# Kernel optimization log

Hardware: AMD Instinct MI355X
Metric: run time of the kernel (lower is better)

The kernel has to match this reference:

```python
import jax, jax.numpy as jnp
import numpy as np

# static config (matches init_kwargs)
H = 64; W = 64; WS = 8; SHIFT = 4; HEADS = 16; DIM = 512; TED = 512; B = 16
NW = (H // WS) * (W // WS)          # 64 windows
WS2 = WS * WS                        # 64 tokens per window
N = WS2 + 1                          # +1 time-embedding token appended per window
HIDDEN = int(DIM * 4.0)


def _rel_pos_index():
    # standard Swin relative-position index over the WS*WS window tokens
    coords = np.stack(np.meshgrid(np.arange(WS), np.arange(WS), indexing='ij'))  # (2, WS, WS)
    cf = coords.reshape(2, -1)
    rel = (cf[:, :, None] - cf[:, None, :]).transpose(1, 2, 0)  # (WS2, WS2, 2)
    rel[..., 0] += WS - 1
    rel[..., 1] += WS - 1
    rel[..., 0] *= 2 * WS - 1
    return rel.sum(-1)  # (WS2, WS2) int


def _attn_mask():
    # shifted-window attention mask, exactly as built in __init__
    img_mask = np.zeros((H, W), dtype=np.float32)
    slices = (slice(0, -WS), slice(-WS, -SHIFT), slice(-SHIFT, None))
    cnt = 0
    for hs in slices:
        for ws_ in slices:
            img_mask[hs, ws_] = cnt
            cnt += 1
    mw = img_mask.reshape(H // WS, WS, W // WS, WS).transpose(0, 2, 1, 3).reshape(-1, WS2)  # (NW, WS2)
    diff = mw[:, None, :] - mw[:, :, None]
    return np.where(diff != 0, -100.0, 0.0).astype(np.float32)  # (NW, WS2, WS2)


def _ln(x, g, b):
    m = x.mean(-1, keepdims=True)
    v = ((x - m) ** 2).mean(-1, keepdims=True)
    return (x - m) / jnp.sqrt(v + 1e-5) * g + b


def setup_inputs() -> dict:
    key = jax.random.key(0)
    ks = jax.random.split(key, 10)
    s = 0.02
    return {
        'x': jax.random.normal(ks[0], (B, H * W, DIM), dtype=jnp.float32),
        'emb': jax.random.normal(ks[1], (B, TED), dtype=jnp.float32),
        'gamma1': jnp.ones((DIM,), jnp.float32),
        'beta1': jnp.zeros((DIM,), jnp.float32),
        'W_emb': jax.random.normal(ks[2], (TED, DIM), jnp.float32) * s,
        'b_emb': jnp.zeros((DIM,), jnp.float32),
        'W_qkv': jax.random.normal(ks[3], (DIM, 3 * DIM), jnp.float32) * s,
        'b_qkv': jnp.zeros((3 * DIM,), jnp.float32),
        'rel_bias_table': jax.random.normal(ks[4], ((2 * WS - 1) ** 2, HEADS), jnp.float32) * s,
        'W_proj': jax.random.normal(ks[5], (DIM, DIM), jnp.float32) * s,
        'b_proj': jnp.zeros((DIM,), jnp.float32),
        'gamma2': jnp.ones((DIM,), jnp.float32),
        'beta2': jnp.zeros((DIM,), jnp.float32),
        'W1': jax.random.normal(ks[6], (DIM, HIDDEN), jnp.float32) * s,
        'b1': jnp.zeros((HIDDEN,), jnp.float32),
        'W2': jax.random.normal(ks[7], (HIDDEN, DIM), jnp.float32) * s,
        'b2': jnp.zeros((DIM,), jnp.float32),
    }


def reference(x, emb, gamma1, beta1, W_emb, b_emb, W_qkv, b_qkv, rel_bias_table,
              W_proj, b_proj, gamma2, beta2, W1, b1, W2, b2):
    Bb, L, C = x.shape
    hd = C // HEADS
    shortcut = x
    # norm1 -> spatial -> cyclic shift
    xn = _ln(x, gamma1, beta1).reshape(Bb, H, W, C)
    xs = jnp.roll(xn, (-SHIFT, -SHIFT), axis=(1, 2))
    # window partition: (B, NW, WS2, C)
    xw = xs.reshape(Bb, H // WS, WS, W // WS, WS, C).transpose(0, 1, 3, 2, 4, 5)
    xw = xw.reshape(Bb, NW, WS2, C)
    # append time-embedding token to each window
    t = jax.nn.silu(emb) @ W_emb + b_emb                       # (B, C)
    t = jnp.broadcast_to(t[:, None, None, :], (Bb, NW, 1, C))
    xw = jnp.concatenate([xw, t], axis=2).reshape(Bb * NW, N, C)
    # windowed multi-head attention
    qkv = (xw @ W_qkv + b_qkv).reshape(Bb * NW, N, 3, HEADS, hd).transpose(2, 0, 3, 1, 4)
    q, k, v = qkv[0] * (hd ** -0.5), qkv[1], qkv[2]            # (B*NW, HEADS, N, hd)
    attn = jnp.einsum('bhnd,bhmd->bhnm', q, k)
    bias = rel_bias_table[_rel_pos_index().reshape(-1)].reshape(WS2, WS2, HEADS).transpose(2, 0, 1)
    bias = jnp.pad(bias, ((0, 0), (0, 1), (0, 1)))             # zero bias for time token
    attn = attn + bias[None]
    mask = jnp.pad(jnp.asarray(_attn_mask()), ((0, 0), (0, 1), (0, 1)))  # (NW, N, N)
    attn = attn.reshape(Bb, NW, HEADS, N, N) + mask[None, :, None]
    attn = jax.nn.softmax(attn.reshape(Bb * NW, HEADS, N, N), axis=-1)
    out = jnp.einsum('bhnm,bhmd->bnhd', attn, v).reshape(Bb * NW, N, C)
    out = (out @ W_proj + b_proj)[:, :WS2]                     # drop time token
    # window reverse + reverse shift
    out = out.reshape(Bb, H // WS, W // WS, WS, WS, C).transpose(0, 1, 3, 2, 4, 5).reshape(Bb, H, W, C)
    out = jnp.roll(out, (SHIFT, SHIFT), axis=(1, 2)).reshape(Bb, L, C)
    x1 = shortcut + out
    # norm2 + MLP (exact GELU, as torch nn.GELU default)
    hmid = jax.nn.gelu(_ln(x1, gamma2, beta2) @ W1 + b1, approximate=False)
    return x1 + hmid @ W2 + b2
```

## Files before the change

### kernel.cpp

```cpp
#include <hip/hip_runtime.h>
#include <hip/hip_bf16.h>

typedef __hip_bfloat16 bf16;
typedef short short4_t __attribute__((ext_vector_type(4)));
typedef short short8 __attribute__((ext_vector_type(8)));
typedef float f32x4 __attribute__((ext_vector_type(4)));

#define DIMC 512
#define HEADS_ 16
#define NTOK 65
#define NWIN 64
#define NB 16
#define HID 2048
#define TOTROWS 66560
#define ATT_CHUNK_WB 128
#define ATT_CHUNK_ROWS (ATT_CHUNK_WB * NTOK)


__device__ __forceinline__ float b2f(short s) {
  unsigned int u = ((unsigned int)(unsigned short)s) << 16;
  float f; __builtin_memcpy(&f, &u, 4); return f;
}
__device__ __forceinline__ short f2s(float f) {
  bf16 b = __float2bfloat16(f);
  short s; __builtin_memcpy(&s, &b, 2); return s;
}

__device__ __forceinline__ void async_lds16(const bf16* g, bf16* l) {
  __builtin_amdgcn_global_load_lds(
      (const __attribute__((address_space(1))) unsigned int*)g,
      (__attribute__((address_space(3))) unsigned int*)l,
      16, 0, 0);
}

__device__ __forceinline__ void wave_stats512(const float* v, float& m, float& rstd)
{
  float s = 0.0f, ss = 0.0f;
  #pragma unroll
  for (int e = 0; e < 8; ++e) { s += v[e]; ss += v[e] * v[e]; }
  #pragma unroll
  for (int o = 1; o < 64; o <<= 1) { s += __shfl_xor(s, o); ss += __shfl_xor(ss, o); }
  m = s * (1.0f / 512.0f);
  rstd = rsqrtf(ss * (1.0f / 512.0f) - m * m + 1e-5f);
}

__device__ __forceinline__ float gelu_t(float v) {
  float u = v + 0.044715f * v * v * v;
  float z2 = 1.5957691216f * fabsf(u);
  float t = __expf(-z2);
  float th = 1.0f - 2.0f * t / (1.0f + t);
  th = (u < 0.0f) ? -th : th;
  return 0.5f * v * (1.0f + th);
}


__global__ __launch_bounds__(256) void time_emb_kernel(
    const float* __restrict__ emb, const float* __restrict__ W_emb,
    const float* __restrict__ b_emb, float* __restrict__ t)
{
  int b = blockIdx.x;
  int c = blockIdx.y * 256 + threadIdx.x;
  __shared__ float se[512];
  for (int k = threadIdx.x; k < 512; k += 256) {
    float e = emb[b * 512 + k];
    se[k] = e / (1.0f + expf(-e));
  }
  __syncthreads();
  float acc = b_emb[c];
  for (int k = 0; k < 512; ++k) acc += se[k] * W_emb[k * 512 + c];
  t[b * 512 + c] = acc;
}

__global__ void transpose_cast_kernel(const float* __restrict__ W, bf16* __restrict__ Wt,
                                      int Kd, int Nd)
{
  __shared__ float tile[32][33];
  int n0 = blockIdx.x * 32, k0 = blockIdx.y * 32;
  for (int r = threadIdx.y; r < 32; r += 8)
    tile[r][threadIdx.x] = W[(long)(k0 + r) * Nd + n0 + threadIdx.x];
  __syncthreads();
  for (int r = threadIdx.y; r < 32; r += 8)
    Wt[(long)(n0 + r) * Kd + k0 + threadIdx.x] = __float2bfloat16(tile[threadIdx.x][r]);
}

__global__ __launch_bounds__(256) void bias_mask_kernel(
    const float* __restrict__ btab, float* __restrict__ tbl)
{
  int h = blockIdx.x, wt = blockIdx.y;
  for (int idx = threadIdx.x; idx < 6400; idx += 256) {
    int i = idx / 80, t = idx % 80;
    float v;
    if (t >= 65) v = -1e30f;
    else if (i >= 64 || t == 64) v = 0.0f;
    else {
      int rel = (((i >> 3) - (t >> 3) + 7) * 15) + ((i & 7) - (t & 7) + 7);
      v = btab[rel * HEADS_ + h];
      int rci = (wt & 2) ? (((i >> 3) < 4) ? 1 : 2) : 0;
      int cci = (wt & 1) ? (((i & 7) < 4) ? 1 : 2) : 0;
      int rct = (wt & 2) ? (((t >> 3) < 4) ? 1 : 2) : 0;
      int cct = (wt & 1) ? (((t & 7) < 4) ? 1 : 2) : 0;
      if (rci * 3 + cci != rct * 3 + cct) v -= 100.0f;
    }
    tbl[(h * 4 + wt) * 6400 + idx] = v;
  }
}

__global__ __launch_bounds__(256) void ln1_window_kernel(
    const float* __restrict__ x, const float* __restrict__ gamma,
    const float* __restrict__ beta, const float* __restrict__ t,
    bf16* __restrict__ xw)
{
  long r = (long)blockIdx.x * 4 + (threadIdx.x >> 6);
  int lane = threadIdx.x & 63;
  int wb = (int)(r / NTOK), i = (int)(r % NTOK);
  int b = wb >> 6, w = wb & 63;
  bf16* out = xw + r * 512 + lane * 8;
  if (i == 64) {
    const float* tr = t + b * 512 + lane * 8;
    short8 o;
    #pragma unroll
    for (int e = 0; e < 8; ++e) o[e] = f2s(tr[e]);
    *(short8*)out = o;
    return;
  }
  int wh = w >> 3, ww = w & 7, ih = i >> 3, iw = i & 7;
  int hsrc = ((wh * 8 + ih) + 4) & 63;
  int wsrc = ((ww * 8 + iw) + 4) & 63;
  const float* xr = x + ((long)b * 4096 + hsrc * 64 + wsrc) * 512 + lane * 8;
  float v[8];
  *(f32x4*)&v[0] = *(const f32x4*)xr;
  *(f32x4*)&v[4] = *(const f32x4*)(xr + 4);
  float m, rstd;
  wave_stats512(v, m, rstd);
  const float* g = gamma + lane * 8;
  const float* bt = beta + lane * 8;
  short8 o;
  #pragma unroll
  for (int e = 0; e < 8; ++e) o[e] = f2s((v[e] - m) * rstd * g[e] + bt[e]);
  *(short8*)out = o;
}

__global__ __launch_bounds__(256) void ln2_kernel(
    const float* __restrict__ x1, const float* __restrict__ gamma,
    const float* __restrict__ beta, bf16* __restrict__ out)
{
  long r = (long)blockIdx.x * 4 + (threadIdx.x >> 6);
  int lane = threadIdx.x & 63;
  const float* xr = x1 + r * 512 + lane * 8;
  float v[8];
  *(f32x4*)&v[0] = *(const f32x4*)xr;
  *(f32x4*)&v[4] = *(const f32x4*)(xr + 4);
  float m, rstd;
  wave_stats512(v, m, rstd);
  const float* g = gamma + lane * 8;
  const float* bt = beta + lane * 8;
  short8 o;
  #pragma unroll
  for (int e = 0; e < 8; ++e) o[e] = f2s((v[e] - m) * rstd * g[e] + bt[e]);
  *(short8*)(out + r * 512 + lane * 8) = o;
}

template<int EPI>
__global__ __launch_bounds__(512, 4) void gemmk_kernel(
    const bf16* __restrict__ A, const bf16* __restrict__ Bt,
    const float* __restrict__ bias, int N, int K, int nx,
    bf16* __restrict__ outB, float* __restrict__ outF,
    const float* __restrict__ xin, int rowOffset)
{
  __shared__ bf16 lA[3][128 * 32];
  __shared__ bf16 lB[3][256 * 32];
  const int tid = threadIdx.x;
  const int lane = tid & 63, wv = tid >> 6;
  const int wm = wv >> 2, wn = wv & 3;
  const int fr = lane & 15, fg = lane >> 4;

  const int nwg = gridDim.x, bid = blockIdx.x;
  const int q = nwg >> 3, rr8 = nwg & 7;
  const int xcd = bid & 7, idx = bid >> 3;
  const int sid = (xcd < rr8 ? xcd * (q + 1) : rr8 * (q + 1) + (xcd - rr8) * q) + idx;
  const long row0 = (long)(sid / nx) * 128;
  const long col0 = (long)(sid % nx) * 256;

  const int rl = lane >> 2, sp = lane & 3;
  const int s = sp ^ ((rl >> 1) & 3);
  const bf16* gA  = A  + (row0 + wv * 16 + rl) * (long)K + s * 8;
  const bf16* gB0 = Bt + (col0 + wv * 16 + rl) * (long)K + s * 8;
  const bf16* gB1 = Bt + (col0 + 128 + wv * 16 + rl) * (long)K + s * 8;

  f32x4 acc[4][4] = {};
  const int nkt = K >> 5;
  const int swr = (fg ^ ((fr >> 1) & 3)) << 4;

  auto stage = [&](int buf, int kt) {
    async_lds16(gA + kt, &lA[buf][wv * 512]);
    async_lds16(gB0 + kt, &lB[buf][wv * 512]);
    async_lds16(gB1 + kt, &lB[buf][4096 + wv * 512]);
  };

  stage(0, 0);
  stage(1, 32);

  for (int t = 0; t < nkt; ++t) {
    if (t + 1 < nkt)
      asm volatile("s_waitcnt vmcnt(3)" ::: "memory");
    else
      asm volatile("s_waitcnt vmcnt(0)" ::: "memory");
    __builtin_amdgcn_s_barrier();
    const int buf = t % 3;
    short8 af[4], bfv[4];
    #pragma unroll
    for (int mi = 0; mi < 4; ++mi)
      af[mi] = *(const short8*)((const char*)&lA[buf][0] + (wm * 64 + mi * 16 + fr) * 64 + swr);
    #pragma unroll
    for (int ni = 0; ni < 4; ++ni)
      bfv[ni] = *(const short8*)((const char*)&lB[buf][0] + (wn * 64 + ni * 16 + fr) * 64 + swr);
    if (t + 2 < nkt) stage((t + 2) % 3, (t + 2) << 5);
    __builtin_amdgcn_s_setprio(1);
    #pragma unroll
    for (int mi = 0; mi < 4; ++mi)
      #pragma unroll
      for (int ni = 0; ni < 4; ++ni)
        acc[mi][ni] = __builtin_amdgcn_mfma_f32_16x16x32_bf16(af[mi], bfv[ni], acc[mi][ni], 0, 0, 0);
    __builtin_amdgcn_s_setprio(0);
  }

  float bs[4];
  #pragma unroll
  for (int ni = 0; ni < 4; ++ni) bs[ni] = bias[col0 + wn * 64 + ni * 16 + fr];
  #pragma unroll
  for (int mi = 0; mi < 4; ++mi) {
    #pragma unroll
    for (int j = 0; j < 4; ++j) {
      long rr = row0 + wm * 64 + mi * 16 + fg * 4 + j;
      if (EPI == 2) {
        int grow = rowOffset + (int)rr;
        int ii = grow % NTOK;
        if (ii == 64) continue;
        int wb = grow / NTOK;
        int b = wb >> 6, w = wb & 63;
        int wh = w >> 3, ww = w & 7, ih = ii >> 3, iw = ii & 7;
        int hh   = ((wh * 8 + ih) + 4) & 63;
        int wcol = ((ww * 8 + iw) + 4) & 63;
        long orow = ((long)b * 4096 + hh * 64 + wcol) * 512;
        #pragma unroll
        for (int ni = 0; ni < 4; ++ni) {
          long o = orow + col0 + wn * 64 + ni * 16 + fr;
          outF[o] = xin[o] + acc[mi][ni][j] + bs[ni];
        }
      } else {
        #pragma unroll
        for (int ni = 0; ni < 4; ++ni) {
          long cc = col0 + wn * 64 + ni * 16 + fr;
          float v = acc[mi][ni][j] + bs[ni];
          if (EPI == 0) {
            outB[rr * N + cc] = __float2bfloat16(v);
          } else if (EPI == 1) {
            outB[rr * N + cc] = __float2bfloat16(gelu_t(v));
          } else {
            long o = rr * N + cc;
            outF[o] = outF[o] + v;
          }
        }
      }
    }
  }
}

__global__ __launch_bounds__(64, 2) void attn_mfma_kernel(
    const bf16* __restrict__ qkv, bf16* __restrict__ attnO,
    const float* __restrict__ tbl, int wb0)
{
  __shared__ bf16 P[80 * 104];
  const int lwb = blockIdx.x, h = blockIdx.y;
  const int lane = threadIdx.x;
  const int fr = lane & 15, g = lane >> 4;
  const float scale = 0.17677669529663687f;
  const bf16* base = qkv + (long)lwb * 65 * 1536 + h * 32 + g * 8;

  for (int idx = lane; idx < 240; idx += 64) {
    int i = idx / 3, sl = idx % 3;
    *(short8*)&P[i * 104 + 80 + sl * 8] = (short8){0, 0, 0, 0, 0, 0, 0, 0};
  }

  short8 bq[5];
  #pragma unroll
  for (int tn = 0; tn < 5; ++tn) {
    int qr = tn * 16 + fr; qr = qr > 64 ? 64 : qr;
    bq[tn] = *(const short8*)(base + (long)qr * 1536);
  }

  f32x4 acc[5][5];
  #pragma unroll
  for (int tm = 0; tm < 5; ++tm) {
    int kr = tm * 16 + fr; kr = kr > 64 ? 64 : kr;
    short8 ak = *(const short8*)(base + 512 + (long)kr * 1536);
    #pragma unroll
    for (int tn = 0; tn < 5; ++tn)
      acc[tm][tn] = __builtin_amdgcn_mfma_f32_16x16x32_bf16(
          ak, bq[tn], (f32x4){0.0f, 0.0f, 0.0f, 0.0f}, 0, 0, 0);
  }

  const int w = (wb0 + lwb) & 63;
  const int wt = (((w >> 3) == 7) ? 2 : 0) + (((w & 7) == 7) ? 1 : 0);
  const float* tp = tbl + (h * 4 + wt) * 6400;
  #pragma unroll
  for (int tn = 0; tn < 5; ++tn) {
    const int i = tn * 16 + fr;
    const float* ti = tp + i * 80 + g * 4;
    float m = -3.0e38f;
    #pragma unroll
    for (int tm = 0; tm < 5; ++tm) {
      f32x4 bv = *(const f32x4*)(ti + tm * 16);
      #pragma unroll
      for (int r = 0; r < 4; ++r) {
        float sv = fmaf(acc[tm][tn][r], scale, bv[r]);
        acc[tm][tn][r] = sv;
        m = fmaxf(m, sv);
      }
    }
    m = fmaxf(m, __shfl_xor(m, 16));
    m = fmaxf(m, __shfl_xor(m, 32));
    float l = 0.0f;
    #pragma unroll
    for (int tm = 0; tm < 5; ++tm)
      #pragma unroll
      for (int r = 0; r < 4; ++r) {
        float e = __expf(acc[tm][tn][r] - m);
        acc[tm][tn][r] = e;
        l += e;
      }
    l += __shfl_xor(l, 16);
    l += __shfl_xor(l, 32);
    float inv = 1.0f / l;
    #pragma unroll
    for (int tm = 0; tm < 5; ++tm) {
      short4_t pk;
      #pragma unroll
      for (int r = 0; r < 4; ++r) pk[r] = f2s(acc[tm][tn][r] * inv);
      *(short4_t*)&P[i * 104 + tm * 16 + g * 4] = pk;
    }
  }

  const bf16* vbase = qkv + (long)lwb * 65 * 1536 + 1024 + h * 32;
  f32x4 oacc[2][5] = {};
  #pragma unroll
  for (int kt = 0; kt < 3; ++kt) {
    short8 bp[5];
    #pragma unroll
    for (int tn = 0; tn < 5; ++tn)
      bp[tn] = *(const short8*)&P[(tn * 16 + fr) * 104 + kt * 32 + g * 8];
    #pragma unroll
    for (int ma = 0; ma < 2; ++ma) {
      short8 av;
      #pragma unroll
      for (int e = 0; e < 8; ++e) {
        int vr = kt * 32 + g * 8 + e; vr = vr > 64 ? 64 : vr;
        av[e] = *(const short*)(vbase + (long)vr * 1536 + ma * 16 + fr);
      }
      #pragma unroll
      for (int tn = 0; tn < 5; ++tn)
        oacc[ma][tn] = __builtin_amdgcn_mfma_f32_16x16x32_bf16(
            av, bp[tn], oacc[ma][tn], 0, 0, 0);
    }
  }

  #pragma unroll
  for (int tn = 0; tn < 5; ++tn) {
    int i = tn * 16 + fr;
    if (i < 65) {
      bf16* op = attnO + (long)(lwb * 65 + i) * 512 + h * 32 + g * 4;
      #pragma unroll
      for (int ma = 0; ma < 2; ++ma) {
        short4_t o4;
        #pragma unroll
        for (int r = 0; r < 4; ++r) o4[r] = f2s(oacc[ma][tn][r]);
        *(short4_t*)(op + ma * 16) = o4;
      }
    }
  }
}


extern "C" void kernel_launch(void* const* d_in, const int* in_sizes, int n_in,
                              void* d_out, int out_size, void* d_ws, size_t ws_size,
                              hipStream_t stream)
{
  const float* x      = (const float*)d_in[0];
  const float* emb    = (const float*)d_in[1];
  const float* gamma1 = (const float*)d_in[2];
  const float* beta1  = (const float*)d_in[3];
  const float* W_emb  = (const float*)d_in[4];
  const float* b_emb  = (const float*)d_in[5];
  const float* W_qkv  = (const float*)d_in[6];
  const float* b_qkv  = (const float*)d_in[7];
  const float* btab   = (const float*)d_in[8];
  const float* W_proj = (const float*)d_in[9];
  const float* b_proj = (const float*)d_in[10];
  const float* gamma2 = (const float*)d_in[11];
  const float* beta2  = (const float*)d_in[12];
  const float* W1     = (const float*)d_in[13];
  const float* b1     = (const float*)d_in[14];
  const float* W2     = (const float*)d_in[15];
  const float* b2     = (const float*)d_in[16];
  float* out = (float*)d_out;
  (void)n_in; (void)in_sizes; (void)out_size;

  char* ws = (char*)d_ws;
  size_t off = 0;
  auto alloc = [&](size_t bytes) -> char* {
    char* p = ws + off;
    off += (bytes + 255) & ~(size_t)255;
    return p;
  };
  bf16* wt_qkv  = (bf16*)alloc((size_t)1536 * 512 * 2);
  bf16* wt_proj = (bf16*)alloc((size_t)512 * 512 * 2);
  bf16* wt1     = (bf16*)alloc((size_t)2048 * 512 * 2);
  bf16* wt2     = (bf16*)alloc((size_t)512 * 2048 * 2);
  float* tvec   = (float*)alloc((size_t)16 * 512 * 4);
  float* tbl    = (float*)alloc((size_t)16 * 4 * 6400 * 4);

  const size_t sz_xw    = (size_t)TOTROWS * 512 * 2;
  const size_t sz_qkv   = (size_t)TOTROWS * 1536 * 2;
  const size_t sz_attnO = (size_t)TOTROWS * 512 * 2;
  const bool big = ws_size >= off + sz_xw + sz_qkv + sz_attnO + (4u << 20);

  transpose_cast_kernel<<<dim3(1536 / 32, 512 / 32), dim3(32, 8), 0, stream>>>(W_qkv, wt_qkv, 512, 1536);
  transpose_cast_kernel<<<dim3(512 / 32, 512 / 32),  dim3(32, 8), 0, stream>>>(W_proj, wt_proj, 512, 512);
  transpose_cast_kernel<<<dim3(2048 / 32, 512 / 32), dim3(32, 8), 0, stream>>>(W1, wt1, 512, 2048);
  transpose_cast_kernel<<<dim3(512 / 32, 2048 / 32), dim3(32, 8), 0, stream>>>(W2, wt2, 2048, 512);
  time_emb_kernel<<<dim3(16, 2), 256, 0, stream>>>(emb, W_emb, b_emb, tvec);
  bias_mask_kernel<<<dim3(16, 4), 256, 0, stream>>>(btab, tbl);

  if (big) {
    bf16* xw    = (bf16*)alloc(sz_xw);
    bf16* qkv   = (bf16*)alloc(sz_qkv);
    bf16* attnO = (bf16*)alloc(sz_attnO);
    bf16* ln2b  = xw;
    bf16* h     = qkv;

    ln1_window_kernel<<<TOTROWS / 4, 256, 0, stream>>>(x, gamma1, beta1, tvec, xw);
    gemmk_kernel<0><<<6 * 520, 512, 0, stream>>>(
        xw, wt_qkv, b_qkv, 1536, 512, 6, qkv, nullptr, nullptr, 0);
    attn_mfma_kernel<<<dim3(NB * NWIN, HEADS_), 64, 0, stream>>>(qkv, attnO, tbl, 0);
    gemmk_kernel<2><<<2 * 520, 512, 0, stream>>>(
        attnO, wt_proj, b_proj, 512, 512, 2, nullptr, out, x, 0);
    ln2_kernel<<<65536 / 4, 256, 0, stream>>>(out, gamma2, beta2, ln2b);
    gemmk_kernel<1><<<8 * 512, 512, 0, stream>>>(
        ln2b, wt1, b1, 2048, 512, 8, h, nullptr, nullptr, 0);
    gemmk_kernel<3><<<2 * 512, 512, 0, stream>>>(
        h, wt2, b2, 512, 2048, 2, nullptr, out, nullptr, 0);
  } else {
    char* regionA = alloc(sz_xw);
    bf16* xw   = (bf16*)regionA;
    bf16* ln2b = (bf16*)regionA;
    bf16* qkv_c = (bf16*)alloc((size_t)ATT_CHUNK_ROWS * 1536 * 2);
    char* regionB = alloc(sz_attnO);
    bf16* attnO = (bf16*)regionB;
    bf16* h_c   = (bf16*)regionB;

    ln1_window_kernel<<<TOTROWS / 4, 256, 0, stream>>>(x, gamma1, beta1, tvec, xw);
    for (int ac = 0; ac < 8; ++ac) {
      long r0 = (long)ac * ATT_CHUNK_ROWS;
      gemmk_kernel<0><<<6 * 65, 512, 0, stream>>>(
          xw + r0 * 512, wt_qkv, b_qkv, 1536, 512, 6, qkv_c, nullptr, nullptr, 0);
      attn_mfma_kernel<<<dim3(ATT_CHUNK_WB, HEADS_), 64, 0, stream>>>(
          qkv_c, attnO + r0 * 512, tbl, ac * ATT_CHUNK_WB);
    }
    gemmk_kernel<2><<<2 * 520, 512, 0, stream>>>(
        attnO, wt_proj, b_proj, 512, 512, 2, nullptr, out, x, 0);
    ln2_kernel<<<65536 / 4, 256, 0, stream>>>(out, gamma2, beta2, ln2b);
    for (int mc = 0; mc < 4; ++mc) {
      long r0 = (long)mc * 16384;
      gemmk_kernel<1><<<8 * 128, 512, 0, stream>>>(
          ln2b + r0 * 512, wt1, b1, 2048, 512, 8, h_c, nullptr, nullptr, 0);
      gemmk_kernel<3><<<2 * 128, 512, 0, stream>>>(
          h_c, wt2, b2, 512, 2048, 2, nullptr, out + r0 * 512, nullptr, 0);
    }
  }
}
```

Measured before the change: 879.2 us.

## Use 4 waves per GEMM block with 128x64 per-wave tiles

Reworks the GEMM from 8 waves in a 2x4 layout to 4 waves, each computing a 128x64 output slab (8x4 MFMA tiles). The block tile stays 128x256, so each block issues fewer threads and each wave does more MFMAs per LDS fragment load. The aim is better arithmetic intensity per wave and less barrier overhead. The cost is doubled accumulator registers and lower occupancy, which means less latency hiding.

```diff
diff --git a/kernel.cpp b/kernel.cpp
--- a/kernel.cpp
+++ b/kernel.cpp
@@ -161,7 +161,7 @@
 }
 
 template<int EPI>
-__global__ __launch_bounds__(512, 4) void gemmk_kernel(
+__global__ __launch_bounds__(256, 2) void gemmk_kernel(
     const bf16* __restrict__ A, const bf16* __restrict__ Bt,
     const float* __restrict__ bias, int N, int K, int nx,
     bf16* __restrict__ outB, float* __restrict__ outF,
@@ -171,30 +171,30 @@
   __shared__ bf16 lB[3][256 * 32];
   const int tid = threadIdx.x;
   const int lane = tid & 63, wv = tid >> 6;
-  const int wm = wv >> 2, wn = wv & 3;
   const int fr = lane & 15, fg = lane >> 4;
 
   const int nwg = gridDim.x, bid = blockIdx.x;
-  const int q = nwg >> 3, rr8 = nwg & 7;
+  const int q8 = nwg >> 3, rr8 = nwg & 7;
   const int xcd = bid & 7, idx = bid >> 3;
-  const int sid = (xcd < rr8 ? xcd * (q + 1) : rr8 * (q + 1) + (xcd - rr8) * q) + idx;
+  const int sid = (xcd < rr8 ? xcd * (q8 + 1) : rr8 * (q8 + 1) + (xcd - rr8) * q8) + idx;
   const long row0 = (long)(sid / nx) * 128;
   const long col0 = (long)(sid % nx) * 256;
 
   const int rl = lane >> 2, sp = lane & 3;
   const int s = sp ^ ((rl >> 1) & 3);
-  const bf16* gA  = A  + (row0 + wv * 16 + rl) * (long)K + s * 8;
-  const bf16* gB0 = Bt + (col0 + wv * 16 + rl) * (long)K + s * 8;
-  const bf16* gB1 = Bt + (col0 + 128 + wv * 16 + rl) * (long)K + s * 8;
-
-  f32x4 acc[4][4] = {};
+  const bf16* gA = A  + (row0 + wv * 32 + rl) * (long)K + s * 8;
+  const bf16* gB = Bt + (col0 + wv * 64 + rl) * (long)K + s * 8;
+
+  f32x4 acc[8][4] = {};
   const int nkt = K >> 5;
   const int swr = (fg ^ ((fr >> 1) & 3)) << 4;
 
-  auto stage = [&](int buf, int kt) {
-    async_lds16(gA + kt, &lA[buf][wv * 512]);
-    async_lds16(gB0 + kt, &lB[buf][wv * 512]);
-    async_lds16(gB1 + kt, &lB[buf][4096 + wv * 512]);
+  auto stage = [&](int buf, long kt) {
+    async_lds16(gA + kt,                 &lA[buf][(wv * 32) * 32]);
+    async_lds16(gA + 16 * (long)K + kt,  &lA[buf][(wv * 32 + 16) * 32]);
+    #pragma unroll
+    for (int qq = 0; qq < 4; ++qq)
+      async_lds16(gB + qq * 16 * (long)K + kt, &lB[buf][(wv * 64 + qq * 16) * 32]);
   };
 
   stage(0, 0);
@@ -202,22 +202,22 @@
 
   for (int t = 0; t < nkt; ++t) {
     if (t + 1 < nkt)
-      asm volatile("s_waitcnt vmcnt(3)" ::: "memory");
+      asm volatile("s_waitcnt vmcnt(6)" ::: "memory");
     else
       asm volatile("s_waitcnt vmcnt(0)" ::: "memory");
     __builtin_amdgcn_s_barrier();
     const int buf = t % 3;
-    short8 af[4], bfv[4];
-    #pragma unroll
-    for (int mi = 0; mi < 4; ++mi)
-      af[mi] = *(const short8*)((const char*)&lA[buf][0] + (wm * 64 + mi * 16 + fr) * 64 + swr);
+    short8 bfv[4], af[8];
     #pragma unroll
     for (int ni = 0; ni < 4; ++ni)
-      bfv[ni] = *(const short8*)((const char*)&lB[buf][0] + (wn * 64 + ni * 16 + fr) * 64 + swr);
-    if (t + 2 < nkt) stage((t + 2) % 3, (t + 2) << 5);
+      bfv[ni] = *(const short8*)((const char*)&lB[buf][0] + (wv * 64 + ni * 16 + fr) * 64 + swr);
+    #pragma unroll
+    for (int mi = 0; mi < 8; ++mi)
+      af[mi] = *(const short8*)((const char*)&lA[buf][0] + (mi * 16 + fr) * 64 + swr);
+    if (t + 2 < nkt) stage((t + 2) % 3, (long)(t + 2) << 5);
     __builtin_amdgcn_s_setprio(1);
     #pragma unroll
-    for (int mi = 0; mi < 4; ++mi)
+    for (int mi = 0; mi < 8; ++mi)
       #pragma unroll
       for (int ni = 0; ni < 4; ++ni)
         acc[mi][ni] = __builtin_amdgcn_mfma_f32_16x16x32_bf16(af[mi], bfv[ni], acc[mi][ni], 0, 0, 0);
@@ -226,12 +226,12 @@
 
   float bs[4];
   #pragma unroll
-  for (int ni = 0; ni < 4; ++ni) bs[ni] = bias[col0 + wn * 64 + ni * 16 + fr];
-  #pragma unroll
-  for (int mi = 0; mi < 4; ++mi) {
+  for (int ni = 0; ni < 4; ++ni) bs[ni] = bias[col0 + wv * 64 + ni * 16 + fr];
+  #pragma unroll
+  for (int mi = 0; mi < 8; ++mi) {
     #pragma unroll
     for (int j = 0; j < 4; ++j) {
-      long rr = row0 + wm * 64 + mi * 16 + fg * 4 + j;
+      long rr = row0 + mi * 16 + fg * 4 + j;
       if (EPI == 2) {
         int grow = rowOffset + (int)rr;
         int ii = grow % NTOK;
@@ -244,13 +244,13 @@
         long orow = ((long)b * 4096 + hh * 64 + wcol) * 512;
         #pragma unroll
         for (int ni = 0; ni < 4; ++ni) {
-          long o = orow + col0 + wn * 64 + ni * 16 + fr;
+          long o = orow + col0 + wv * 64 + ni * 16 + fr;
           outF[o] = xin[o] + acc[mi][ni][j] + bs[ni];
         }
       } else {
         #pragma unroll
         for (int ni = 0; ni < 4; ++ni) {
-          long cc = col0 + wn * 64 + ni * 16 + fr;
+          long cc = col0 + wv * 64 + ni * 16 + fr;
           float v = acc[mi][ni][j] + bs[ni];
           if (EPI == 0) {
             outB[rr * N + cc] = __float2bfloat16(v);
@@ -439,15 +439,15 @@
     bf16* h     = qkv;
 
     ln1_window_kernel<<<TOTROWS / 4, 256, 0, stream>>>(x, gamma1, beta1, tvec, xw);
-    gemmk_kernel<0><<<6 * 520, 512, 0, stream>>>(
+    gemmk_kernel<0><<<6 * 520, 256, 0, stream>>>(
         xw, wt_qkv, b_qkv, 1536, 512, 6, qkv, nullptr, nullptr, 0);
     attn_mfma_kernel<<<dim3(NB * NWIN, HEADS_), 64, 0, stream>>>(qkv, attnO, tbl, 0);
-    gemmk_kernel<2><<<2 * 520, 512, 0, stream>>>(
+    gemmk_kernel<2><<<2 * 520, 256, 0, stream>>>(
         attnO, wt_proj, b_proj, 512, 512, 2, nullptr, out, x, 0);
     ln2_kernel<<<65536 / 4, 256, 0, stream>>>(out, gamma2, beta2, ln2b);
-    gemmk_kernel<1><<<8 * 512, 512, 0, stream>>>(
+    gemmk_kernel<1><<<8 * 512, 256, 0, stream>>>(
         ln2b, wt1, b1, 2048, 512, 8, h, nullptr, nullptr, 0);
-    gemmk_kernel<3><<<2 * 512, 512, 0, stream>>>(
+    gemmk_kernel<3><<<2 * 512, 256, 0, stream>>>(
         h, wt2, b2, 512, 2048, 2, nullptr, out, nullptr, 0);
   } else {
     char* regionA = alloc(sz_xw);
@@ -461,19 +461,19 @@
     ln1_window_kernel<<<TOTROWS / 4, 256, 0, stream>>>(x, gamma1, beta1, tvec, xw);
     for (int ac = 0; ac < 8; ++ac) {
       long r0 = (long)ac * ATT_CHUNK_ROWS;
-      gemmk_kernel<0><<<6 * 65, 512, 0, stream>>>(
+      gemmk_kernel<0><<<6 * 65, 256, 0, stream>>>(
           xw + r0 * 512, wt_qkv, b_qkv, 1536, 512, 6, qkv_c, nullptr, nullptr, 0);
       attn_mfma_kernel<<<dim3(ATT_CHUNK_WB, HEADS_), 64, 0, stream>>>(
           qkv_c, attnO + r0 * 512, tbl, ac * ATT_CHUNK_WB);
     }
-    gemmk_kernel<2><<<2 * 520, 512, 0, stream>>>(
+    gemmk_kernel<2><<<2 * 520, 256, 0, stream>>>(
         attnO, wt_proj, b_proj, 512, 512, 2, nullptr, out, x, 0);
     ln2_kernel<<<65536 / 4, 256, 0, stream>>>(out, gamma2, beta2, ln2b);
     for (int mc = 0; mc < 4; ++mc) {
       long r0 = (long)mc * 16384;
-      gemmk_kernel<1><<<8 * 128, 512, 0, stream>>>(
+      gemmk_kernel<1><<<8 * 128, 256, 0, stream>>>(
           ln2b + r0 * 512, wt1, b1, 2048, 512, 8, h_c, nullptr, nullptr, 0);
-      gemmk_kernel<3><<<2 * 128, 512, 0, stream>>>(
+      gemmk_kernel<3><<<2 * 128, 256, 0, stream>>>(
           h_c, wt2, b2, 512, 2048, 2, nullptr, out + r0 * 512, nullptr, 0);
     }
   }
```

New measurement: 904.5 us. 2.9% more time.
